# Kernel tuning notes

Measured on AMD Instinct MI355X. Metric: run time of the kernel, lower is better.

Reference implementation:

```python
import jax, jax.numpy as jnp
import numpy as np

REGRESS_FACTOR = (0.1, 0.1, 0.2, 0.2)
CLS_THRESH = 0.05


def setup_inputs() -> dict:
    key = jax.random.key(0)
    k1, k2, k3, k4, k5 = jax.random.split(key, 5)
    B, N, C = 8, 49104, 500
    H = W = 512
    imgs = jax.random.normal(k1, (B, 3, H, W), dtype=jnp.float32)
    classifications = jax.random.uniform(k2, (B, N, C), dtype=jnp.float32)
    regressions = jax.random.normal(k3, (B, N, 4), dtype=jnp.float32) * 0.5
    # valid anchors: random centers in-image, sizes in [16, 112)
    ctr = jax.random.uniform(k4, (1, N, 2), dtype=jnp.float32) * W
    wh = jax.random.uniform(k5, (1, N, 2), dtype=jnp.float32) * 96.0 + 16.0
    anchors = jnp.concatenate([ctr - 0.5 * wh, ctr + 0.5 * wh], axis=-1)
    return {"imgs": imgs, "classifications": classifications,
            "regressions": regressions, "anchors": anchors}


def _regress_and_clip(anchors, regressions, img_h, img_w):
    fx, fy, fw, fh = REGRESS_FACTOR
    widths = anchors[..., 2] - anchors[..., 0]
    heights = anchors[..., 3] - anchors[..., 1]
    ctr_x = anchors[..., 0] + 0.5 * widths
    ctr_y = anchors[..., 1] + 0.5 * heights

    dx = regressions[..., 0] * fx
    dy = regressions[..., 1] * fy
    dw = regressions[..., 2] * fw
    dh = regressions[..., 3] * fh

    pred_ctr_x = ctr_x + dx * widths
    pred_ctr_y = ctr_y + dy * heights
    pred_w = jnp.exp(dw) * widths
    pred_h = jnp.exp(dh) * heights

    boxes = jnp.stack([
        pred_ctr_x - 0.5 * pred_w,
        pred_ctr_y - 0.5 * pred_h,
        pred_ctr_x + 0.5 * pred_w,
        pred_ctr_y + 0.5 * pred_h,
    ], axis=-1)  # [B, N, 4]

    # ClipBoxes: clamp to image extent
    lo = jnp.zeros((4,), boxes.dtype)
    hi = jnp.array([img_w, img_h, img_w, img_h], boxes.dtype)
    return jnp.clip(boxes, lo, hi)


def reference(imgs, classifications, regressions, anchors):
    # Per-class max score and class index
    scores = jnp.max(classifications, axis=2)        # [B, N]
    cls_idx = jnp.argmax(classifications, axis=2)    # [B, N]
    mask = scores > CLS_THRESH                       # [B, N]

    img_h, img_w = imgs.shape[2], imgs.shape[3]
    boxes = _regress_and_clip(anchors, regressions, img_h, img_w)  # [B, N, 4]

    # The torch module compacts per image (ragged); jit-compatible equivalent:
    # return dense arrays with the selection mask applied.
    m = mask.astype(boxes.dtype)
    boxes_m = boxes * m[..., None]
    scores_m = scores * m
    return boxes_m, scores_m, cls_idx, mask
```

## Files before the change

### kernel.cpp

```cpp
#include <hip/hip_runtime.h>
#include <math.h>

#define CLS_THRESH 0.05f

__global__ __launch_bounds__(256) void infer_transform_kernel(
    const float* __restrict__ cls,
    const float* __restrict__ reg,
    const float* __restrict__ anch,
    float* __restrict__ out,
    int B, int N, int C, float img_w, float img_h)
{
    const int wavesPerBlock = blockDim.x >> 6;
    const int wave = threadIdx.x >> 6;
    const int lane = threadIdx.x & 63;
    const long long rows = (long long)B * N;
    const long long row  = (long long)blockIdx.x * wavesPerBlock + wave;
    if (row >= rows) return;

    const int n = (int)(row % (long long)N);
    const float* __restrict__ crow = cls + row * (long long)C;

    float best = -INFINITY;
    int   bidx = 0x7fffffff;
    const int nvec = C >> 2;
    for (int i = lane; i < nvec; i += 64) {
        const float4 v = reinterpret_cast<const float4*>(crow)[i];
        const int base = i << 2;
        if (v.x > best) { best = v.x; bidx = base;     }
        if (v.y > best) { best = v.y; bidx = base + 1; }
        if (v.z > best) { best = v.z; bidx = base + 2; }
        if (v.w > best) { best = v.w; bidx = base + 3; }
    }
    for (int i = (nvec << 2) + lane; i < C; i += 64) {
        const float v = crow[i];
        if (v > best) { best = v; bidx = i; }
    }

    #pragma unroll
    for (int off = 32; off >= 1; off >>= 1) {
        const float ov = __shfl_xor(best, off, 64);
        const int   oi = __shfl_xor(bidx, off, 64);
        if (ov > best || (ov == best && oi < bidx)) { best = ov; bidx = oi; }
    }

    if (lane == 0) {
        const float4 rg = reinterpret_cast<const float4*>(reg)[row];
        const float4 an = reinterpret_cast<const float4*>(anch)[n];

        const float w  = an.z - an.x;
        const float h  = an.w - an.y;
        const float cx = an.x + 0.5f * w;
        const float cy = an.y + 0.5f * h;

        const float dx = rg.x * 0.1f;
        const float dy = rg.y * 0.1f;
        const float dw = rg.z * 0.2f;
        const float dh = rg.w * 0.2f;

        const float pcx = cx + dx * w;
        const float pcy = cy + dy * h;
        const float pw  = expf(dw) * w;
        const float ph  = expf(dh) * h;

        float x1 = pcx - 0.5f * pw;
        float y1 = pcy - 0.5f * ph;
        float x2 = pcx + 0.5f * pw;
        float y2 = pcy + 0.5f * ph;

        x1 = fminf(fmaxf(x1, 0.0f), img_w);
        y1 = fminf(fmaxf(y1, 0.0f), img_h);
        x2 = fminf(fmaxf(x2, 0.0f), img_w);
        y2 = fminf(fmaxf(y2, 0.0f), img_h);

        const float m = (best > CLS_THRESH) ? 1.0f : 0.0f;

        reinterpret_cast<float4*>(out)[row] = make_float4(x1 * m, y1 * m, x2 * m, y2 * m);
        out[rows * 4 + row] = best * m;
        out[rows * 5 + row] = (float)bidx;
        out[rows * 6 + row] = m;
    }
}

extern "C" void kernel_launch(void* const* d_in, const int* in_sizes, int n_in,
                              void* d_out, int out_size, void* d_ws, size_t ws_size,
                              hipStream_t stream) {
    const float* cls  = (const float*)d_in[1];
    const float* reg  = (const float*)d_in[2];
    const float* anch = (const float*)d_in[3];
    float* out = (float*)d_out;

    const int N  = in_sizes[3] / 4;
    const int BN = in_sizes[2] / 4;
    const int B  = BN / N;
    const int C  = (int)((long long)in_sizes[1] / BN);
    const long long hw = (long long)in_sizes[0] / (3LL * B);
    const int W = (int)(sqrt((double)hw) + 0.5);
    const float img_w = (float)W, img_h = (float)W;

    const int wavesPerBlock = 4;
    const int blocks = (BN + wavesPerBlock - 1) / wavesPerBlock;
    infer_transform_kernel<<<blocks, 256, 0, stream>>>(cls, reg, anch, out,
                                                       B, N, C, img_w, img_h);
}
```

Before: 1.005 ms.

## Use persistent grid-stride waves processing two rows per iteration with unrolled loads

```diff
diff --git a/kernel.cpp b/kernel.cpp
--- a/kernel.cpp
+++ b/kernel.cpp
@@ -2,82 +2,114 @@
 #include <math.h>
 
 #define CLS_THRESH 0.05f
+#define NEG_INF (-__builtin_inff())
+
+__device__ __forceinline__ void upd4(float& b, int& bi, const float4 v, const int base) {
+    if (v.x > b) { b = v.x; bi = base;     }
+    if (v.y > b) { b = v.y; bi = base + 1; }
+    if (v.z > b) { b = v.z; bi = base + 2; }
+    if (v.w > b) { b = v.w; bi = base + 3; }
+}
+
+__device__ __forceinline__ void epilogue(
+    float best, int bidx, int row, int N, int rows,
+    const float* __restrict__ reg, const float* __restrict__ anch,
+    float* __restrict__ out, float img_w, float img_h)
+{
+    const int n = row % N;
+    const float4 rg = reinterpret_cast<const float4*>(reg)[row];
+    const float4 an = reinterpret_cast<const float4*>(anch)[n];
+
+    const float w  = an.z - an.x;
+    const float h  = an.w - an.y;
+    const float cx = an.x + 0.5f * w;
+    const float cy = an.y + 0.5f * h;
+
+    const float pcx = cx + rg.x * 0.1f * w;
+    const float pcy = cy + rg.y * 0.1f * h;
+    const float pw  = expf(rg.z * 0.2f) * w;
+    const float ph  = expf(rg.w * 0.2f) * h;
+
+    float x1 = fminf(fmaxf(pcx - 0.5f * pw, 0.0f), img_w);
+    float y1 = fminf(fmaxf(pcy - 0.5f * ph, 0.0f), img_h);
+    float x2 = fminf(fmaxf(pcx + 0.5f * pw, 0.0f), img_w);
+    float y2 = fminf(fmaxf(pcy + 0.5f * ph, 0.0f), img_h);
+
+    const float m = (best > CLS_THRESH) ? 1.0f : 0.0f;
+
+    reinterpret_cast<float4*>(out)[row] = make_float4(x1 * m, y1 * m, x2 * m, y2 * m);
+    out[(long long)rows * 4 + row] = best * m;
+    out[(long long)rows * 5 + row] = (float)bidx;
+    out[(long long)rows * 6 + row] = m;
+}
 
 __global__ __launch_bounds__(256) void infer_transform_kernel(
     const float* __restrict__ cls,
     const float* __restrict__ reg,
     const float* __restrict__ anch,
     float* __restrict__ out,
-    int B, int N, int C, float img_w, float img_h)
+    int N, int C, int rows, float img_w, float img_h)
 {
-    const int wavesPerBlock = blockDim.x >> 6;
-    const int wave = threadIdx.x >> 6;
     const int lane = threadIdx.x & 63;
-    const long long rows = (long long)B * N;
-    const long long row  = (long long)blockIdx.x * wavesPerBlock + wave;
-    if (row >= rows) return;
+    const int wid  = blockIdx.x * (blockDim.x >> 6) + (threadIdx.x >> 6);
+    const int nW   = gridDim.x * (blockDim.x >> 6);
+    const int nvec = C >> 2;
 
-    const int n = (int)(row % (long long)N);
-    const float* __restrict__ crow = cls + row * (long long)C;
+    if (nvec <= 128 && (C & 3) == 0) {
+        for (int r0 = wid; r0 < rows; r0 += 2 * nW) {
+            const int  r1   = r0 + nW;
+            const bool has1 = r1 < rows;
+            const float4* c0 = reinterpret_cast<const float4*>(cls + (long long)r0 * C);
+            const float4* c1 = reinterpret_cast<const float4*>(cls + (long long)(has1 ? r1 : r0) * C);
 
-    float best = -INFINITY;
-    int   bidx = 0x7fffffff;
-    const int nvec = C >> 2;
-    for (int i = lane; i < nvec; i += 64) {
-        const float4 v = reinterpret_cast<const float4*>(crow)[i];
-        const int base = i << 2;
-        if (v.x > best) { best = v.x; bidx = base;     }
-        if (v.y > best) { best = v.y; bidx = base + 1; }
-        if (v.z > best) { best = v.z; bidx = base + 2; }
-        if (v.w > best) { best = v.w; bidx = base + 3; }
-    }
-    for (int i = (nvec << 2) + lane; i < C; i += 64) {
-        const float v = crow[i];
-        if (v > best) { best = v; bidx = i; }
-    }
+            const float4 a0 = c0[lane];
+            const float4 a1 = c1[lane];
+            const bool hi = (lane + 64) < nvec;
+            float4 d0, d1;
+            if (hi) { d0 = c0[lane + 64]; d1 = c1[lane + 64]; }
 
-    #pragma unroll
-    for (int off = 32; off >= 1; off >>= 1) {
-        const float ov = __shfl_xor(best, off, 64);
-        const int   oi = __shfl_xor(bidx, off, 64);
-        if (ov > best || (ov == best && oi < bidx)) { best = ov; bidx = oi; }
-    }
+            float b0 = NEG_INF, b1 = NEG_INF;
+            int   j0 = 0,       j1 = 0;
+            upd4(b0, j0, a0, lane << 2);
+            upd4(b1, j1, a1, lane << 2);
+            if (hi) {
+                upd4(b0, j0, d0, (lane + 64) << 2);
+                upd4(b1, j1, d1, (lane + 64) << 2);
+            }
 
-    if (lane == 0) {
-        const float4 rg = reinterpret_cast<const float4*>(reg)[row];
-        const float4 an = reinterpret_cast<const float4*>(anch)[n];
+            #pragma unroll
+            for (int off = 32; off >= 1; off >>= 1) {
+                const float o0v = __shfl_xor(b0, off, 64);
+                const int   o0j = __shfl_xor(j0, off, 64);
+                const float o1v = __shfl_xor(b1, off, 64);
+                const int   o1j = __shfl_xor(j1, off, 64);
+                if (o0v > b0 || (o0v == b0 && o0j < j0)) { b0 = o0v; j0 = o0j; }
+                if (o1v > b1 || (o1v == b1 && o1j < j1)) { b1 = o1v; j1 = o1j; }
+            }
 
-        const float w  = an.z - an.x;
-        const float h  = an.w - an.y;
-        const float cx = an.x + 0.5f * w;
-        const float cy = an.y + 0.5f * h;
-
-        const float dx = rg.x * 0.1f;
-        const float dy = rg.y * 0.1f;
-        const float dw = rg.z * 0.2f;
-        const float dh = rg.w * 0.2f;
-
-        const float pcx = cx + dx * w;
-        const float pcy = cy + dy * h;
-        const float pw  = expf(dw) * w;
-        const float ph  = expf(dh) * h;
-
-        float x1 = pcx - 0.5f * pw;
-        float y1 = pcy - 0.5f * ph;
-        float x2 = pcx + 0.5f * pw;
-        float y2 = pcy + 0.5f * ph;
-
-        x1 = fminf(fmaxf(x1, 0.0f), img_w);
-        y1 = fminf(fmaxf(y1, 0.0f), img_h);
-        x2 = fminf(fmaxf(x2, 0.0f), img_w);
-        y2 = fminf(fmaxf(y2, 0.0f), img_h);
-
-        const float m = (best > CLS_THRESH) ? 1.0f : 0.0f;
-
-        reinterpret_cast<float4*>(out)[row] = make_float4(x1 * m, y1 * m, x2 * m, y2 * m);
-        out[rows * 4 + row] = best * m;
-        out[rows * 5 + row] = (float)bidx;
-        out[rows * 6 + row] = m;
+            if (lane == 0) {
+                epilogue(b0, j0, r0, N, rows, reg, anch, out, img_w, img_h);
+                if (has1) epilogue(b1, j1, r1, N, rows, reg, anch, out, img_w, img_h);
+            }
+        }
+    } else {
+        for (int row = wid; row < rows; row += nW) {
+            const float* crow = cls + (long long)row * C;
+            float b = NEG_INF; int j = 0;
+            for (int i = lane; i < nvec; i += 64)
+                upd4(b, j, reinterpret_cast<const float4*>(crow)[i], i << 2);
+            for (int i = (nvec << 2) + lane; i < C; i += 64) {
+                const float v = crow[i];
+                if (v > b) { b = v; j = i; }
+            }
+            #pragma unroll
+            for (int off = 32; off >= 1; off >>= 1) {
+                const float ov = __shfl_xor(b, off, 64);
+                const int   oj = __shfl_xor(j, off, 64);
+                if (ov > b || (ov == b && oj < j)) { b = ov; j = oj; }
+            }
+            if (lane == 0) epilogue(b, j, row, N, rows, reg, anch, out, img_w, img_h);
+        }
     }
 }
 
@@ -89,16 +121,18 @@
     const float* anch = (const float*)d_in[3];
     float* out = (float*)d_out;
 
-    const int N  = in_sizes[3] / 4;
-    const int BN = in_sizes[2] / 4;
-    const int B  = BN / N;
-    const int C  = (int)((long long)in_sizes[1] / BN);
+    const int N    = in_sizes[3] / 4;
+    const int rows = in_sizes[2] / 4;
+    const int B    = rows / N;
+    const int C    = (int)((long long)in_sizes[1] / rows);
     const long long hw = (long long)in_sizes[0] / (3LL * B);
     const int W = (int)(sqrt((double)hw) + 0.5);
     const float img_w = (float)W, img_h = (float)W;
 
-    const int wavesPerBlock = 4;
-    const int blocks = (BN + wavesPerBlock - 1) / wavesPerBlock;
+    int blocks = 2048;
+    const int max_needed = (rows + 3) / 4;
+    if (blocks > max_needed) blocks = max_needed;
+
     infer_transform_kernel<<<blocks, 256, 0, stream>>>(cls, reg, anch, out,
-                                                       B, N, C, img_w, img_h);
+                                                       N, C, rows, img_w, img_h);
 }
```

New measurement: 1.038 ms. 3.3% more time.
